# Kernel tuning notes

Hardware: AMD Instinct MI355X
Metric: run time of the kernel (lower is better)

## Reference

```python
import jax, jax.numpy as jnp
import numpy as np

B, D, C = 2048, 1024, 8192


def setup_inputs() -> dict:
    key = jax.random.key(0)
    k1, k2, k3 = jax.random.split(key, 3)
    x = jax.random.normal(k1, (B, D), dtype=jnp.float32)
    y = jax.random.randint(k2, (B,), 0, C)
    centroids = jax.random.normal(k3, (C, D), dtype=jnp.float32)
    return {"x": x, "y": y, "centroids": centroids}


def reference(x, y, centroids):
    x2 = jnp.sum(x * x, axis=-1, keepdims=True)          # (B, 1)
    c2 = jnp.sum(centroids * centroids, axis=-1)          # (C,)
    logits = -(x2 + c2[None, :] - 2.0 * (x @ centroids.T))  # (B, C)
    decisions = jnp.argmax(logits, axis=1)                # nearest centroid
    score = jnp.mean((decisions == y).astype(jnp.float32))
    # CrossEntropyLoss(distances, y)
    logp = jax.nn.log_softmax(logits, axis=-1)
    loss = -jnp.mean(jnp.take_along_axis(logp, y[:, None], axis=1))
    return loss, score
```

## Files before the change

### kernel.cpp

```cpp
#include <hip/hip_runtime.h>
#include <cstdint>

#define MDIM 2048
#define KDIM 1024
#define CDIM 8192
#define BM 128
#define BN 128
#define BK 32
#define NCHUNK (2 * (CDIM / BN))

typedef __attribute__((ext_vector_type(8))) __bf16 bf16x8;
typedef __attribute__((ext_vector_type(4))) float f32x4;

__device__ __forceinline__ unsigned short f2bf(float f) {
  unsigned u = __float_as_uint(f);
  u += 0x7fffu + ((u >> 16) & 1u);
  return (unsigned short)(u >> 16);
}

__device__ __forceinline__ void async_ld16(const void* g, void* l) {
  __builtin_amdgcn_global_load_lds(
      (__attribute__((address_space(1))) void*)(g),
      (__attribute__((address_space(3))) void*)(l),
      16, 0, 0);
}

__global__ __launch_bounds__(256) void prep(const float* __restrict__ x,
                                            const float* __restrict__ cent,
                                            unsigned short* __restrict__ xb,
                                            unsigned short* __restrict__ cb,
                                            float* __restrict__ c2) {
  const int wave = threadIdx.x >> 6, lane = threadIdx.x & 63;
  const int row = blockIdx.x * 4 + wave;
  if (row < MDIM) {
    const float4* src = (const float4*)(x + (size_t)row * KDIM);
    ushort4* dst = (ushort4*)(xb + (size_t)row * KDIM);
    float4 v[4];
#pragma unroll
    for (int i = 0; i < 4; ++i) v[i] = src[lane + 64 * i];
#pragma unroll
    for (int i = 0; i < 4; ++i) {
      ushort4 o;
      o.x = f2bf(v[i].x); o.y = f2bf(v[i].y); o.z = f2bf(v[i].z); o.w = f2bf(v[i].w);
      dst[lane + 64 * i] = o;
    }
  } else {
    const int r = row - MDIM;
    const float4* src = (const float4*)(cent + (size_t)r * KDIM);
    ushort4* dst = (ushort4*)(cb + (size_t)r * KDIM);
    float4 v[4];
#pragma unroll
    for (int i = 0; i < 4; ++i) v[i] = src[lane + 64 * i];
    float p = 0.f;
#pragma unroll
    for (int i = 0; i < 4; ++i) {
      ushort4 o;
      o.x = f2bf(v[i].x); o.y = f2bf(v[i].y); o.z = f2bf(v[i].z); o.w = f2bf(v[i].w);
      dst[lane + 64 * i] = o;
      p += v[i].x * v[i].x + v[i].y * v[i].y + v[i].z * v[i].z + v[i].w * v[i].w;
    }
    for (int d = 32; d; d >>= 1) p += __shfl_down(p, d, 64);
    if (lane == 0) c2[r] = p;
  }
}

__global__ __launch_bounds__(256) void gemm_reduce(
    const unsigned short* __restrict__ Ab, const unsigned short* __restrict__ Bb,
    const float* __restrict__ c2,
    float* __restrict__ pm, float* __restrict__ pl, int* __restrict__ pidx) {
  __shared__ __align__(16) unsigned short As[BM * BK];
  __shared__ __align__(16) unsigned short Bs[BN * BK];
  const int tid = threadIdx.x;
  const int wave = tid >> 6, lane = tid & 63;
  const int wm = wave >> 1, wn = wave & 1;
  const int bn = blockIdx.x, bm = blockIdx.y;
  const int quad = lane >> 4, c16 = lane & 15;

  f32x4 acc[4][4] = {};

  const int srow = lane >> 2;
  const int scol = (lane & 3) * 8;
  const unsigned short* ag = Ab + (size_t)(bm * BM + wave * 32 + srow) * KDIM + scol;
  const unsigned short* bg = Bb + (size_t)(bn * BN + wave * 32 + srow) * KDIM + scol;
  unsigned short* asl = &As[(wave * 32) * BK];
  unsigned short* bsl = &Bs[(wave * 32) * BK];

  for (int k0 = 0; k0 < KDIM; k0 += BK) {
    async_ld16(ag + k0, asl);
    async_ld16(ag + k0 + 16 * KDIM, asl + 16 * BK);
    async_ld16(bg + k0, bsl);
    async_ld16(bg + k0 + 16 * KDIM, bsl + 16 * BK);
    __syncthreads();
    bf16x8 a[4], b[4];
#pragma unroll
    for (int mt = 0; mt < 4; ++mt)
      a[mt] = *(const bf16x8*)&As[(wm * 64 + mt * 16 + c16) * BK + quad * 8];
#pragma unroll
    for (int nt = 0; nt < 4; ++nt)
      b[nt] = *(const bf16x8*)&Bs[(wn * 64 + nt * 16 + c16) * BK + quad * 8];
#pragma unroll
    for (int mt = 0; mt < 4; ++mt)
#pragma unroll
      for (int nt = 0; nt < 4; ++nt)
        acc[mt][nt] = __builtin_amdgcn_mfma_f32_16x16x32_bf16(a[mt], b[nt], acc[mt][nt], 0, 0, 0);
    __syncthreads();
  }

  const int colbase = bn * BN + wn * 64;
  float c2v[4];
#pragma unroll
  for (int nt = 0; nt < 4; ++nt) c2v[nt] = c2[colbase + nt * 16 + c16];

  const int chunk = bn * 2 + wn;
#pragma unroll
  for (int mt = 0; mt < 4; ++mt) {
#pragma unroll
    for (int r = 0; r < 4; ++r) {
      float sv[4];
#pragma unroll
      for (int nt = 0; nt < 4; ++nt) sv[nt] = 2.0f * acc[mt][nt][r] - c2v[nt];
      float m = sv[0];
      int idx = colbase + c16;
#pragma unroll
      for (int nt = 1; nt < 4; ++nt) {
        if (sv[nt] > m) { m = sv[nt]; idx = colbase + nt * 16 + c16; }
      }
      for (int d = 1; d < 16; d <<= 1) {
        const float om = __shfl_xor(m, d, 64);
        const int oi = __shfl_xor(idx, d, 64);
        if (om > m || (om == m && oi < idx)) { m = om; idx = oi; }
      }
      float l = __expf(sv[0] - m) + __expf(sv[1] - m) + __expf(sv[2] - m) + __expf(sv[3] - m);
      for (int d = 1; d < 16; d <<= 1) l += __shfl_xor(l, d, 64);
      if (c16 == 0) {
        const int row = bm * BM + wm * 64 + mt * 16 + quad * 4 + r;
        pm[(size_t)row * NCHUNK + chunk] = m;
        pl[(size_t)row * NCHUNK + chunk] = l;
        pidx[(size_t)row * NCHUNK + chunk] = idx;
      }
    }
  }
}

__global__ __launch_bounds__(128) void combine_kernel(
    const float* __restrict__ pm, const float* __restrict__ pl,
    const int* __restrict__ pidx, const float* __restrict__ x,
    const float* __restrict__ cent, const float* __restrict__ c2,
    const int* __restrict__ y,
    float* __restrict__ loss_part, float* __restrict__ corr_part) {
  const int row = blockIdx.x, t = threadIdx.x;
  const int yc = y[row];

  float m = pm[(size_t)row * NCHUNK + t];
  float l = pl[(size_t)row * NCHUNK + t];
  int idx = pidx[(size_t)row * NCHUNK + t];

  const float4* xa = (const float4*)(x + (size_t)row * KDIM) + t * 2;
  const float4* ca = (const float4*)(cent + (size_t)yc * KDIM) + t * 2;
  const float4 a0 = xa[0], a1 = xa[1], b0 = ca[0], b1 = ca[1];
  float dot = a0.x * b0.x + a0.y * b0.y + a0.z * b0.z + a0.w * b0.w
            + a1.x * b1.x + a1.y * b1.y + a1.z * b1.z + a1.w * b1.w;

  float M = m;
  int gidx = idx;
  for (int d = 1; d < 64; d <<= 1) {
    const float om = __shfl_xor(M, d, 64);
    const int oi = __shfl_xor(gidx, d, 64);
    const float od = __shfl_xor(dot, d, 64);
    if (om > M || (om == M && oi < gidx)) { M = om; gidx = oi; }
    dot += od;
  }
  __shared__ float sm[2], sd[2];
  __shared__ int si[2];
  if ((t & 63) == 0) { sm[t >> 6] = M; si[t >> 6] = gidx; sd[t >> 6] = dot; }
  __syncthreads();
  const float Mg = fmaxf(sm[0], sm[1]);
  float lr = l * __expf(m - Mg);
  for (int d = 1; d < 64; d <<= 1) lr += __shfl_xor(lr, d, 64);
  __shared__ float sl[2];
  if ((t & 63) == 0) sl[t >> 6] = lr;
  __syncthreads();
  if (t == 0) {
    const float L = sl[0] + sl[1];
    int g;
    if (sm[1] > sm[0] || (sm[1] == sm[0] && si[1] < si[0])) g = si[1]; else g = si[0];
    const float sy = 2.0f * (sd[0] + sd[1]) - c2[yc];
    loss_part[row] = __logf(L) + Mg - sy;
    corr_part[row] = (g == yc) ? 1.f : 0.f;
  }
}

__global__ __launch_bounds__(256) void finalize(const float* __restrict__ loss_part,
                                                const float* __restrict__ corr_part,
                                                float* __restrict__ out) {
  const int t = threadIdx.x;
  float s0 = 0.f, s1 = 0.f;
  for (int i = t; i < MDIM; i += 256) { s0 += loss_part[i]; s1 += corr_part[i]; }
  for (int d = 32; d; d >>= 1) {
    s0 += __shfl_down(s0, d, 64);
    s1 += __shfl_down(s1, d, 64);
  }
  __shared__ float r0[4], r1[4];
  if ((t & 63) == 0) { r0[t >> 6] = s0; r1[t >> 6] = s1; }
  __syncthreads();
  if (t == 0) {
    out[0] = (r0[0] + r0[1] + r0[2] + r0[3]) * (1.0f / MDIM);
    out[1] = (r1[0] + r1[1] + r1[2] + r1[3]) * (1.0f / MDIM);
  }
}

extern "C" void kernel_launch(void* const* d_in, const int* in_sizes, int n_in,
                              void* d_out, int out_size, void* d_ws, size_t ws_size,
                              hipStream_t stream) {
  const float* x = (const float*)d_in[0];
  const int* y = (const int*)d_in[1];
  const float* cent = (const float*)d_in[2];
  float* out = (float*)d_out;

  char* ws = (char*)d_ws;
  const size_t OFF_XB = 0;
  const size_t OFF_CB = OFF_XB + (size_t)MDIM * KDIM * 2;
  const size_t OFF_C2 = OFF_CB + (size_t)CDIM * KDIM * 2;
  const size_t OFF_PM = OFF_C2 + (size_t)CDIM * 4;
  const size_t OFF_PL = OFF_PM + (size_t)NCHUNK * MDIM * 4;
  const size_t OFF_PI = OFF_PL + (size_t)NCHUNK * MDIM * 4;
  const size_t OFF_LP = OFF_PI + (size_t)NCHUNK * MDIM * 4;
  const size_t OFF_CP = OFF_LP + (size_t)MDIM * 4;
  const size_t NEED = OFF_CP + (size_t)MDIM * 4;
  if (ws_size < NEED) return;

  unsigned short* xb = (unsigned short*)(ws + OFF_XB);
  unsigned short* cb = (unsigned short*)(ws + OFF_CB);
  float* c2 = (float*)(ws + OFF_C2);
  float* pm = (float*)(ws + OFF_PM);
  float* pl = (float*)(ws + OFF_PL);
  int* pidx = (int*)(ws + OFF_PI);
  float* loss_part = (float*)(ws + OFF_LP);
  float* corr_part = (float*)(ws + OFF_CP);

  prep<<<(MDIM + CDIM) / 4, 256, 0, stream>>>(x, cent, xb, cb, c2);
  gemm_reduce<<<dim3(CDIM / BN, MDIM / BM), 256, 0, stream>>>(xb, cb, c2, pm, pl, pidx);
  combine_kernel<<<MDIM, 128, 0, stream>>>(pm, pl, pidx, x, cent, c2, y, loss_part, corr_part);
  finalize<<<1, 256, 0, stream>>>(loss_part, corr_part, out);
}
```

Before: 157.7 us.

## Fuse bf16 conversion and centroid norms into GEMM, drop prep kernel

Removes the separate prep kernel. The GEMM now loads fp32 x and centroids directly, converts them to bf16 in registers and writes them into padded LDS tiles (row stride 40 to reduce bank conflicts). It also accumulates centroid squared norms during the K loop and keeps them in shared memory. The combine kernel computes ||c_y||^2 itself, and loads are register-prefetched one K step ahead. This saves the extra bf16 write and read pass and one launch, but the GEMM now reads twice the bytes per tile, each x and centroid tile is re-read and re-converted by many blocks, and the async global-to-LDS loads are dropped.

```diff
diff --git a/kernel.cpp b/kernel.cpp
--- a/kernel.cpp
+++ b/kernel.cpp
@@ -7,97 +7,74 @@
 #define BM 128
 #define BN 128
 #define BK 32
+#define SROW 40
 #define NCHUNK (2 * (CDIM / BN))
 
 typedef __attribute__((ext_vector_type(8))) __bf16 bf16x8;
 typedef __attribute__((ext_vector_type(4))) float f32x4;
-
-__device__ __forceinline__ unsigned short f2bf(float f) {
-  unsigned u = __float_as_uint(f);
-  u += 0x7fffu + ((u >> 16) & 1u);
-  return (unsigned short)(u >> 16);
-}
-
-__device__ __forceinline__ void async_ld16(const void* g, void* l) {
-  __builtin_amdgcn_global_load_lds(
-      (__attribute__((address_space(1))) void*)(g),
-      (__attribute__((address_space(3))) void*)(l),
-      16, 0, 0);
-}
-
-__global__ __launch_bounds__(256) void prep(const float* __restrict__ x,
-                                            const float* __restrict__ cent,
-                                            unsigned short* __restrict__ xb,
-                                            unsigned short* __restrict__ cb,
-                                            float* __restrict__ c2) {
-  const int wave = threadIdx.x >> 6, lane = threadIdx.x & 63;
-  const int row = blockIdx.x * 4 + wave;
-  if (row < MDIM) {
-    const float4* src = (const float4*)(x + (size_t)row * KDIM);
-    ushort4* dst = (ushort4*)(xb + (size_t)row * KDIM);
-    float4 v[4];
-#pragma unroll
-    for (int i = 0; i < 4; ++i) v[i] = src[lane + 64 * i];
-#pragma unroll
-    for (int i = 0; i < 4; ++i) {
-      ushort4 o;
-      o.x = f2bf(v[i].x); o.y = f2bf(v[i].y); o.z = f2bf(v[i].z); o.w = f2bf(v[i].w);
-      dst[lane + 64 * i] = o;
-    }
-  } else {
-    const int r = row - MDIM;
-    const float4* src = (const float4*)(cent + (size_t)r * KDIM);
-    ushort4* dst = (ushort4*)(cb + (size_t)r * KDIM);
-    float4 v[4];
-#pragma unroll
-    for (int i = 0; i < 4; ++i) v[i] = src[lane + 64 * i];
-    float p = 0.f;
-#pragma unroll
-    for (int i = 0; i < 4; ++i) {
-      ushort4 o;
-      o.x = f2bf(v[i].x); o.y = f2bf(v[i].y); o.z = f2bf(v[i].z); o.w = f2bf(v[i].w);
-      dst[lane + 64 * i] = o;
-      p += v[i].x * v[i].x + v[i].y * v[i].y + v[i].z * v[i].z + v[i].w * v[i].w;
-    }
-    for (int d = 32; d; d >>= 1) p += __shfl_down(p, d, 64);
-    if (lane == 0) c2[r] = p;
-  }
-}
-
-__global__ __launch_bounds__(256) void gemm_reduce(
-    const unsigned short* __restrict__ Ab, const unsigned short* __restrict__ Bb,
-    const float* __restrict__ c2,
+typedef __attribute__((ext_vector_type(8))) unsigned short u16x8;
+
+__device__ __forceinline__ unsigned short f2bf_rna(float f) {
+  return (unsigned short)((__float_as_uint(f) + 0x8000u) >> 16);
+}
+
+__device__ __forceinline__ u16x8 pack_bf16(float4 a, float4 b) {
+  u16x8 r;
+  r[0] = f2bf_rna(a.x); r[1] = f2bf_rna(a.y); r[2] = f2bf_rna(a.z); r[3] = f2bf_rna(a.w);
+  r[4] = f2bf_rna(b.x); r[5] = f2bf_rna(b.y); r[6] = f2bf_rna(b.z); r[7] = f2bf_rna(b.w);
+  return r;
+}
+
+__global__ __launch_bounds__(256) void gemm_fused(
+    const float* __restrict__ X, const float* __restrict__ Cf,
     float* __restrict__ pm, float* __restrict__ pl, int* __restrict__ pidx) {
-  __shared__ __align__(16) unsigned short As[BM * BK];
-  __shared__ __align__(16) unsigned short Bs[BN * BK];
+  __shared__ __align__(16) unsigned short As[BM * SROW];
+  __shared__ __align__(16) unsigned short Bs[BN * SROW];
+  __shared__ float c2s[BN];
   const int tid = threadIdx.x;
   const int wave = tid >> 6, lane = tid & 63;
   const int wm = wave >> 1, wn = wave & 1;
   const int bn = blockIdx.x, bm = blockIdx.y;
   const int quad = lane >> 4, c16 = lane & 15;
 
+  const int sr = tid >> 1;
+  const int sh = tid & 1;
+  const float* ag = X  + (size_t)(bm * BM + sr) * KDIM + sh * 16;
+  const float* bg = Cf + (size_t)(bn * BN + sr) * KDIM + sh * 16;
+  unsigned short* aw = &As[sr * SROW + sh * 16];
+  unsigned short* bw = &Bs[sr * SROW + sh * 16];
+
   f32x4 acc[4][4] = {};
-
-  const int srow = lane >> 2;
-  const int scol = (lane & 3) * 8;
-  const unsigned short* ag = Ab + (size_t)(bm * BM + wave * 32 + srow) * KDIM + scol;
-  const unsigned short* bg = Bb + (size_t)(bn * BN + wave * 32 + srow) * KDIM + scol;
-  unsigned short* asl = &As[(wave * 32) * BK];
-  unsigned short* bsl = &Bs[(wave * 32) * BK];
+  float sq = 0.f;
+
+  float4 av[4], bv[4];
+#pragma unroll
+  for (int j = 0; j < 4; ++j) { av[j] = ((const float4*)ag)[j]; bv[j] = ((const float4*)bg)[j]; }
 
   for (int k0 = 0; k0 < KDIM; k0 += BK) {
-    async_ld16(ag + k0, asl);
-    async_ld16(ag + k0 + 16 * KDIM, asl + 16 * BK);
-    async_ld16(bg + k0, bsl);
-    async_ld16(bg + k0 + 16 * KDIM, bsl + 16 * BK);
+#pragma unroll
+    for (int j = 0; j < 4; ++j)
+      sq += bv[j].x * bv[j].x + bv[j].y * bv[j].y + bv[j].z * bv[j].z + bv[j].w * bv[j].w;
+    *(u16x8*)(aw)     = pack_bf16(av[0], av[1]);
+    *(u16x8*)(aw + 8) = pack_bf16(av[2], av[3]);
+    *(u16x8*)(bw)     = pack_bf16(bv[0], bv[1]);
+    *(u16x8*)(bw + 8) = pack_bf16(bv[2], bv[3]);
     __syncthreads();
+
+    if (k0 + BK < KDIM) {
+      const float* an = ag + k0 + BK;
+      const float* bnx = bg + k0 + BK;
+#pragma unroll
+      for (int j = 0; j < 4; ++j) { av[j] = ((const float4*)an)[j]; bv[j] = ((const float4*)bnx)[j]; }
+    }
+
     bf16x8 a[4], b[4];
 #pragma unroll
     for (int mt = 0; mt < 4; ++mt)
-      a[mt] = *(const bf16x8*)&As[(wm * 64 + mt * 16 + c16) * BK + quad * 8];
+      a[mt] = *(const bf16x8*)&As[(wm * 64 + mt * 16 + c16) * SROW + quad * 8];
 #pragma unroll
     for (int nt = 0; nt < 4; ++nt)
-      b[nt] = *(const bf16x8*)&Bs[(wn * 64 + nt * 16 + c16) * BK + quad * 8];
+      b[nt] = *(const bf16x8*)&Bs[(wn * 64 + nt * 16 + c16) * SROW + quad * 8];
 #pragma unroll
     for (int mt = 0; mt < 4; ++mt)
 #pragma unroll
@@ -106,10 +83,14 @@
     __syncthreads();
   }
 
+  sq += __shfl_xor(sq, 1, 64);
+  if (sh == 0) c2s[sr] = sq;
+  __syncthreads();
+
   const int colbase = bn * BN + wn * 64;
   float c2v[4];
 #pragma unroll
-  for (int nt = 0; nt < 4; ++nt) c2v[nt] = c2[colbase + nt * 16 + c16];
+  for (int nt = 0; nt < 4; ++nt) c2v[nt] = c2s[wn * 64 + nt * 16 + c16];
 
   const int chunk = bn * 2 + wn;
 #pragma unroll
@@ -145,8 +126,7 @@
 __global__ __launch_bounds__(128) void combine_kernel(
     const float* __restrict__ pm, const float* __restrict__ pl,
     const int* __restrict__ pidx, const float* __restrict__ x,
-    const float* __restrict__ cent, const float* __restrict__ c2,
-    const int* __restrict__ y,
+    const float* __restrict__ cent, const int* __restrict__ y,
     float* __restrict__ loss_part, float* __restrict__ corr_part) {
   const int row = blockIdx.x, t = threadIdx.x;
   const int yc = y[row];
@@ -160,6 +140,8 @@
   const float4 a0 = xa[0], a1 = xa[1], b0 = ca[0], b1 = ca[1];
   float dot = a0.x * b0.x + a0.y * b0.y + a0.z * b0.z + a0.w * b0.w
             + a1.x * b1.x + a1.y * b1.y + a1.z * b1.z + a1.w * b1.w;
+  float cc = b0.x * b0.x + b0.y * b0.y + b0.z * b0.z + b0.w * b0.w
+           + b1.x * b1.x + b1.y * b1.y + b1.z * b1.z + b1.w * b1.w;
 
   float M = m;
   int gidx = idx;
@@ -167,12 +149,14 @@
     const float om = __shfl_xor(M, d, 64);
     const int oi = __shfl_xor(gidx, d, 64);
     const float od = __shfl_xor(dot, d, 64);
+    const float oc = __shfl_xor(cc, d, 64);
     if (om > M || (om == M && oi < gidx)) { M = om; gidx = oi; }
     dot += od;
-  }
-  __shared__ float sm[2], sd[2];
+    cc += oc;
+  }
+  __shared__ float sm[2], sd[2], sc[2];
   __shared__ int si[2];
-  if ((t & 63) == 0) { sm[t >> 6] = M; si[t >> 6] = gidx; sd[t >> 6] = dot; }
+  if ((t & 63) == 0) { sm[t >> 6] = M; si[t >> 6] = gidx; sd[t >> 6] = dot; sc[t >> 6] = cc; }
   __syncthreads();
   const float Mg = fmaxf(sm[0], sm[1]);
   float lr = l * __expf(m - Mg);
@@ -184,7 +168,7 @@
     const float L = sl[0] + sl[1];
     int g;
     if (sm[1] > sm[0] || (sm[1] == sm[0] && si[1] < si[0])) g = si[1]; else g = si[0];
-    const float sy = 2.0f * (sd[0] + sd[1]) - c2[yc];
+    const float sy = 2.0f * (sd[0] + sd[1]) - (sc[0] + sc[1]);
     loss_part[row] = __logf(L) + Mg - sy;
     corr_part[row] = (g == yc) ? 1.f : 0.f;
   }
@@ -218,10 +202,7 @@
   float* out = (float*)d_out;
 
   char* ws = (char*)d_ws;
-  const size_t OFF_XB = 0;
-  const size_t OFF_CB = OFF_XB + (size_t)MDIM * KDIM * 2;
-  const size_t OFF_C2 = OFF_CB + (size_t)CDIM * KDIM * 2;
-  const size_t OFF_PM = OFF_C2 + (size_t)CDIM * 4;
+  const size_t OFF_PM = 0;
   const size_t OFF_PL = OFF_PM + (size_t)NCHUNK * MDIM * 4;
   const size_t OFF_PI = OFF_PL + (size_t)NCHUNK * MDIM * 4;
   const size_t OFF_LP = OFF_PI + (size_t)NCHUNK * MDIM * 4;
@@ -229,17 +210,13 @@
   const size_t NEED = OFF_CP + (size_t)MDIM * 4;
   if (ws_size < NEED) return;
 
-  unsigned short* xb = (unsigned short*)(ws + OFF_XB);
-  unsigned short* cb = (unsigned short*)(ws + OFF_CB);
-  float* c2 = (float*)(ws + OFF_C2);
   float* pm = (float*)(ws + OFF_PM);
   float* pl = (float*)(ws + OFF_PL);
   int* pidx = (int*)(ws + OFF_PI);
   float* loss_part = (float*)(ws + OFF_LP);
   float* corr_part = (float*)(ws + OFF_CP);
 
-  prep<<<(MDIM + CDIM) / 4, 256, 0, stream>>>(x, cent, xb, cb, c2);
-  gemm_reduce<<<dim3(CDIM / BN, MDIM / BM), 256, 0, stream>>>(xb, cb, c2, pm, pl, pidx);
-  combine_kernel<<<MDIM, 128, 0, stream>>>(pm, pl, pidx, x, cent, c2, y, loss_part, corr_part);
+  gemm_fused<<<dim3(CDIM / BN, MDIM / BM), 256, 0, stream>>>(x, cent, pm, pl, pidx);
+  combine_kernel<<<MDIM, 128, 0, stream>>>(pm, pl, pidx, x, cent, y, loss_part, corr_part);
   finalize<<<1, 256, 0, stream>>>(loss_part, corr_part, out);
 }
```

Measured after the change: 172.8 us. 1.1x slower.
